# Kernel tuning notes

Measured on AMD Instinct MI355X. Metric: run time of the kernel, lower is better.

The kernel has to match this reference:

```python
import jax, jax.numpy as jnp
import numpy as np

NEG_SLOPE = 0.2  # PyG GATConv default


def gat_conv(x, src, dst, W_src, W_dst, att_src, att_dst, bias, heads, ch, n_nodes):
    """One PyG-style GATConv with self-loops already included in (src, dst).
    Returns [N, heads*ch] (concat over heads)."""
    xs = (x @ W_src).reshape(n_nodes, heads, ch)  # source-side transform (messages)
    xd = (x @ W_dst).reshape(n_nodes, heads, ch)  # dest-side transform (attention only)
    a_s = jnp.sum(xs * att_src, axis=-1)  # [N, H]
    a_d = jnp.sum(xd * att_dst, axis=-1)  # [N, H]
    e = jax.nn.leaky_relu(a_s[src] + a_d[dst], NEG_SLOPE)  # [E, H]
    # segment softmax over edges grouped by destination node
    m = jax.ops.segment_max(e, dst, num_segments=n_nodes)  # [N, H]
    ex = jnp.exp(e - m[dst])
    denom = jax.ops.segment_sum(ex, dst, num_segments=n_nodes)  # [N, H]
    alpha = ex / denom[dst]  # [E, H]
    # weighted scatter-aggregate of source messages
    out = jax.ops.segment_sum(xs[src] * alpha[:, :, None], dst, num_segments=n_nodes)
    return out.reshape(n_nodes, heads * ch) + bias


def setup_inputs() -> dict:
    key = jax.random.key(0)
    ks = jax.random.split(key, 12)
    N, F, E = 50000, 128, 400000
    H, C1, C2 = 4, 64, 64
    x = jax.random.normal(ks[0], (N, F), dtype=jnp.float32)
    edge_index = jax.random.randint(ks[1], (2, E), 0, N, dtype=jnp.int64)
    g = lambda k, shape, fan_in: jax.random.normal(k, shape, dtype=jnp.float32) * (1.0 / np.sqrt(fan_in))
    return {
        "x": x,
        "edge_index": edge_index,
        "W1_src": g(ks[2], (F, H * C1), F),
        "W1_dst": g(ks[3], (F, H * C1), F),
        "att1_src": g(ks[4], (H, C1), C1),
        "att1_dst": g(ks[5], (H, C1), C1),
        "b1": jnp.zeros((H * C1,), dtype=jnp.float32),
        "W2_src": g(ks[6], (H * C1, C2), H * C1),
        "W2_dst": g(ks[7], (H * C1, C2), H * C1),
        "att2_src": g(ks[8], (1, C2), C2),
        "att2_dst": g(ks[9], (1, C2), C2),
        "b2": jnp.zeros((C2,), dtype=jnp.float32),
    }


def reference(x, edge_index, W1_src, W1_dst, att1_src, att1_dst, b1,
              W2_src, W2_dst, att2_src, att2_dst, b2):
    N = x.shape[0]
    loop = jnp.arange(N, dtype=edge_index.dtype)
    src = jnp.concatenate([edge_index[0], loop])  # add_self_loops=True
    dst = jnp.concatenate([edge_index[1], loop])
    H, C1 = att1_src.shape
    C2 = att2_src.shape[1]
    h = gat_conv(x, src, dst, W1_src, W1_dst, att1_src, att1_dst, b1, H, C1, N)
    h = jax.nn.relu(h)
    # dropout is identity in eval mode
    out = gat_conv(h, src, dst, W2_src, W2_dst, att2_src, att2_dst, b2, 1, C2, N)
    return out
```

## Files before the change

### kernel.cpp

```cpp
#include <hip/hip_runtime.h>


static inline int cdiv(int a, int b) { return (a + b - 1) / b; }

typedef __attribute__((ext_vector_type(8))) short short8;
typedef __attribute__((ext_vector_type(4))) float floatx4;

__device__ __forceinline__ float bf2f(unsigned short u) {
  return __uint_as_float(((unsigned int)u) << 16);
}
__device__ __forceinline__ unsigned short f2bf(float f) {
  unsigned int u = __float_as_uint(f);
  unsigned int r = (u + 0x7FFFu + ((u >> 16) & 1u)) >> 16;
  return (unsigned short)r;
}
__device__ __forceinline__ float ldv(const void* p, int i, int bf) {
  return bf ? bf2f(((const unsigned short*)p)[i]) : ((const float*)p)[i];
}
#define NEG_INF (-__builtin_inff())

__global__ void fill_out_kernel(float* __restrict__ out, int n, float val) {
  int t = blockIdx.x * blockDim.x + threadIdx.x;
  if (t < n) out[t] = val;
}

__device__ void block_probes(const unsigned short* xu, const unsigned int* eu,
                             int& bf, int& e64) {
  __shared__ int cc, ce;
  if (threadIdx.x == 0) { cc = 0; ce = 0; }
  __syncthreads();
  int l0 = 0, l1 = 0;
  for (int i = threadIdx.x; i < 1024; i += 256) {
    int e = (xu[2 * i] >> 7) & 0xFF;
    if (e >= 100 && e <= 141) l0++;
    if (eu[2 * i + 1] == 0u) l1++;
  }
  atomicAdd(&cc, l0); atomicAdd(&ce, l1);
  __syncthreads();
  bf = cc > 512 ? 1 : 0;
  e64 = ce > 512 ? 1 : 0;
}

__global__ void prep_edges(const unsigned short* __restrict__ xu,
                           const void* __restrict__ EI, int E, int EP, int Nn,
                           const void* __restrict__ W1s, const void* __restrict__ W1d,
                           const void* __restrict__ a1s, const void* __restrict__ a1d,
                           const void* __restrict__ W2s, const void* __restrict__ W2d,
                           const void* __restrict__ a2s, const void* __restrict__ a2d,
                           const void* __restrict__ b1, const void* __restrict__ b2,
                           unsigned short* __restrict__ W1c,
                           unsigned short* __restrict__ W2sT,
                           unsigned short* __restrict__ W1ext,
                           float* __restrict__ v2s, float* __restrict__ v2d,
                           float* __restrict__ b1f, float* __restrict__ b2f,
                           int* __restrict__ srcI, int* __restrict__ dstI,
                           int* __restrict__ posE,
                           int* __restrict__ deg) {
  const int b = blockIdx.x, t = threadIdx.x;
  int bf, e64;
  block_probes(xu, (const unsigned int*)EI, bf, e64);
  if (b < 128) {
    int i = b * 256 + t;
    W1c[i] = f2bf(ldv(W1s, i, bf));
  } else if (b < 192) {
    int i = (b - 128) * 256 + t;
    int k = i >> 6, col = i & 63;
    W2sT[col * 256 + k] = f2bf(ldv(W2s, i, bf));
  } else if (b < 198) {
    const int lane = t & 63, w = t >> 6;
    const int g = lane >> 3, ll = lane & 7;
    const int base = (b - 192) * 256 + w * 64 + g;
#pragma unroll
    for (int r = 0; r < 8; ++r) {
      const int d = base + r * 8;
      const void *W, *A;
      int wo, ao;
      if (d < 1024) {
        int k = d >> 3, q = d & 7, h = q & 3;
        W = (q < 4) ? W1s : W1d;
        A = (q < 4) ? a1s : a1d;
        wo = k * 256 + h * 64;
        ao = h * 64;
      } else {
        int e = d - 1024, k = e & 255;
        W = (e < 256) ? W2s : W2d;
        A = (e < 256) ? a2s : a2d;
        wo = k * 64;
        ao = 0;
      }
      float p;
      if (bf) {
        uint4 wv = *(const uint4*)((const unsigned short*)W + wo + ll * 8);
        uint4 av = *(const uint4*)((const unsigned short*)A + ao + ll * 8);
        p  = bf2f((unsigned short)(wv.x & 0xFFFF)) * bf2f((unsigned short)(av.x & 0xFFFF));
        p += bf2f((unsigned short)(wv.x >> 16))    * bf2f((unsigned short)(av.x >> 16));
        p += bf2f((unsigned short)(wv.y & 0xFFFF)) * bf2f((unsigned short)(av.y & 0xFFFF));
        p += bf2f((unsigned short)(wv.y >> 16))    * bf2f((unsigned short)(av.y >> 16));
        p += bf2f((unsigned short)(wv.z & 0xFFFF)) * bf2f((unsigned short)(av.z & 0xFFFF));
        p += bf2f((unsigned short)(wv.z >> 16))    * bf2f((unsigned short)(av.z >> 16));
        p += bf2f((unsigned short)(wv.w & 0xFFFF)) * bf2f((unsigned short)(av.w & 0xFFFF));
        p += bf2f((unsigned short)(wv.w >> 16))    * bf2f((unsigned short)(av.w >> 16));
      } else {
        float4 w0 = *(const float4*)((const float*)W + wo + ll * 8);
        float4 w1 = *(const float4*)((const float*)W + wo + ll * 8 + 4);
        float4 a0 = *(const float4*)((const float*)A + ao + ll * 8);
        float4 a1 = *(const float4*)((const float*)A + ao + ll * 8 + 4);
        p = w0.x * a0.x + w0.y * a0.y + w0.z * a0.z + w0.w * a0.w +
            w1.x * a1.x + w1.y * a1.y + w1.z * a1.z + w1.w * a1.w;
      }
      p += __shfl_xor(p, 1);
      p += __shfl_xor(p, 2);
      p += __shfl_xor(p, 4);
      if (ll == 0) {
        if (d < 1024) {
          int k = d >> 3, q = d & 7;
          W1ext[k * 16 + q] = f2bf(p);
          W1ext[k * 16 + 8 + q] = 0;
        } else {
          int e = d - 1024, k = e & 255;
          if (e < 256) v2s[k] = p; else v2d[k] = p;
        }
      }
    }
  } else if (b == 198) {
    b1f[t] = ldv(b1, t, bf);
    if (t < 64) b2f[t] = ldv(b2, t, bf);
  } else {
    int i = (b - 199) * 256 + t;
    if (i < EP) {
      int s, d;
      if (i < E) {
        if (e64) {
          const unsigned int* p = (const unsigned int*)EI;
          s = (int)p[2 * (size_t)i];
          d = (int)p[2 * ((size_t)E + i)];
        } else {
          const int* p = (const int*)EI;
          s = p[i]; d = p[E + i];
        }
      } else { s = i - E; d = s; }
      if ((unsigned)s >= (unsigned)Nn) s = 0;
      if ((unsigned)d >= (unsigned)Nn) d = 0;
      srcI[i] = s; dstI[i] = d;
      posE[i] = atomicAdd(&deg[d], 1);
    }
  }
}

__global__ __launch_bounds__(256) void scan_gemm(
    const void* __restrict__ X, const unsigned short* __restrict__ xu,
    const int* __restrict__ deg, int* __restrict__ rowst,
    int* __restrict__ scanflag, int nb,
    const unsigned short* __restrict__ W1c, const unsigned short* __restrict__ W1ext,
    unsigned short* __restrict__ xs1, float* __restrict__ A1, int N) {
  __shared__ __align__(16) unsigned short smem[9 * 16 * 136];
  const int t = threadIdx.x;
  if (blockIdx.x < nb) {
    const int c = blockIdx.x;
    int* ssc = (int*)smem;
    int i = c * 256 + t;
    int v = (i < N) ? deg[i] : 0;
    ssc[t] = v;
    __syncthreads();
    for (int off = 1; off < 256; off <<= 1) {
      int add = (t >= off) ? ssc[t - off] : 0;
      __syncthreads();
      ssc[t] += add;
      __syncthreads();
    }
    int incl = ssc[t];
    if (t == 255) atomicExch(&scanflag[c], ssc[255] + 1);
    __syncthreads();
    int pre = 0;
    if (t < c) {
      int f;
      while ((f = atomicAdd(&scanflag[t], 0)) == 0) {}
      pre = f - 1;
    }
    int* s2 = ssc + 256;
    s2[t] = pre;
    __syncthreads();
    for (int off = 128; off; off >>= 1) {
      if (t < off) s2[t] += s2[t + off];
      __syncthreads();
    }
    if (i < N) rowst[i] = s2[0] + incl - v;
    return;
  }
  __shared__ int pcc;
  if (t == 0) pcc = 0;
  __syncthreads();
  {
    int l0 = 0;
    for (int i = t; i < 1024; i += 256) {
      int e = (xu[2 * i] >> 7) & 0xFF;
      if (e >= 100 && e <= 141) l0++;
    }
    atomicAdd(&pcc, l0);
  }
  __syncthreads();
  const int bf = pcc > 512 ? 1 : 0;
  unsigned short* Wlds = smem;
  const int lane = t & 63, wid = t >> 6;
  const int quad = lane >> 4, m16 = lane & 15;
  const int r0b = (blockIdx.x - nb) * 64;
  const int r0 = r0b + wid * 16;
  const int arow = min(r0 + m16, N - 1);
  short8 af[4];
  if (bf) {
    const uint4* Xr = (const uint4*)((const unsigned int*)X + (size_t)arow * 64);
#pragma unroll
    for (int ks = 0; ks < 4; ++ks)
      af[ks] = __builtin_bit_cast(short8, Xr[ks * 4 + quad]);
  } else {
    const float* Xr = (const float*)X + (size_t)arow * 128;
#pragma unroll
    for (int ks = 0; ks < 4; ++ks) {
      short8 v;
#pragma unroll
      for (int j = 0; j < 8; ++j) v[j] = (short)f2bf(Xr[ks * 32 + quad * 8 + j]);
      af[ks] = v;
    }
  }
  floatx4 accs[9];
  if (t < 144) {
    for (int k0 = 0; k0 < 128; k0 += 4) {
      unsigned int u0, u1;
      if (t < 128) {
        const unsigned short* p = W1c + (size_t)k0 * 256 + t;
        u0 = (unsigned int)p[0] | ((unsigned int)p[256] << 16);
        u1 = (unsigned int)p[512] | ((unsigned int)p[768] << 16);
      } else {
        const unsigned short* p = W1ext + (size_t)k0 * 16 + (t - 128);
        u0 = (unsigned int)p[0] | ((unsigned int)p[16] << 16);
        u1 = (unsigned int)p[32] | ((unsigned int)p[48] << 16);
      }
      *(uint2*)&Wlds[t * 136 + k0] = make_uint2(u0, u1);
    }
  }
  __syncthreads();
#pragma unroll
  for (int ct = 0; ct < 9; ++ct) {
    floatx4 acc = {0.f, 0.f, 0.f, 0.f};
    const unsigned short* wl = &Wlds[(ct * 16 + m16) * 136];
#pragma unroll
    for (int ks = 0; ks < 4; ++ks) {
      short8 bfv = *(const short8*)(wl + ks * 32 + quad * 8);
      acc = __builtin_amdgcn_mfma_f32_16x16x32_bf16(af[ks], bfv, acc, 0, 0, 0);
    }
    accs[ct] = acc;
  }
  __syncthreads();
  if (m16 < 8) {
#pragma unroll
    for (int r = 0; r < 4; ++r) {
      int row = r0 + quad * 4 + r;
      if (row < N) A1[(size_t)row * 8 + m16] = accs[8][r];
    }
  }
#pragma unroll
  for (int ct = 0; ct < 8; ++ct)
#pragma unroll
    for (int r = 0; r < 4; ++r)
      Wlds[(wid * 16 + quad * 4 + r) * 136 + ct * 16 + m16] = f2bf(accs[ct][r]);
  __syncthreads();
#pragma unroll
  for (int it = 0; it < 4; ++it) {
    int lrow = it * 16 + (t >> 4);
    int grow = r0b + lrow;
    if (grow < N) {
      uint4 v = *(const uint4*)&Wlds[lrow * 136 + (t & 15) * 8];
      *(uint4*)(xs1 + (size_t)grow * 256 + (t & 15) * 8) = v;
    }
  }
  __syncthreads();
  if (t < 128) {
    for (int k0 = 0; k0 < 128; k0 += 4) {
      const unsigned short* p = W1c + (size_t)k0 * 256 + 128 + t;
      unsigned int u0 = (unsigned int)p[0] | ((unsigned int)p[256] << 16);
      unsigned int u1 = (unsigned int)p[512] | ((unsigned int)p[768] << 16);
      *(uint2*)&Wlds[t * 136 + k0] = make_uint2(u0, u1);
    }
  }
  __syncthreads();
#pragma unroll
  for (int ct = 0; ct < 8; ++ct) {
    floatx4 acc = {0.f, 0.f, 0.f, 0.f};
    const unsigned short* wl = &Wlds[(ct * 16 + m16) * 136];
#pragma unroll
    for (int ks = 0; ks < 4; ++ks) {
      short8 bfv = *(const short8*)(wl + ks * 32 + quad * 8);
      acc = __builtin_amdgcn_mfma_f32_16x16x32_bf16(af[ks], bfv, acc, 0, 0, 0);
    }
    accs[ct] = acc;
  }
  __syncthreads();
#pragma unroll
  for (int ct = 0; ct < 8; ++ct)
#pragma unroll
    for (int r = 0; r < 4; ++r)
      Wlds[(wid * 16 + quad * 4 + r) * 136 + ct * 16 + m16] = f2bf(accs[ct][r]);
  __syncthreads();
#pragma unroll
  for (int it = 0; it < 4; ++it) {
    int lrow = it * 16 + (t >> 4);
    int grow = r0b + lrow;
    if (grow < N) {
      uint4 v = *(const uint4*)&Wlds[lrow * 136 + (t & 15) * 8];
      *(uint4*)(xs1 + (size_t)grow * 256 + 128 + (t & 15) * 8) = v;
    }
  }
}

__global__ void fill_srcS(const int* __restrict__ srcI, const int* __restrict__ dstI,
                          const int* __restrict__ posE, int EP,
                          const int* __restrict__ rowst, int* __restrict__ srcS) {
  int t = blockIdx.x * blockDim.x + threadIdx.x;
  if (t >= EP) return;
  int d = dstI[t];
  srcS[rowst[d] + posE[t]] = srcI[t];
}

__global__ __launch_bounds__(256) void node1_merged(
    const int* __restrict__ rowst, const int* __restrict__ deg,
    const int* __restrict__ srcS,
    const float* __restrict__ A1, const unsigned short* __restrict__ xs1,
    const float* __restrict__ b1f, const unsigned short* __restrict__ W2sT,
    const float* __restrict__ v2s, const float* __restrict__ v2d,
    unsigned short* __restrict__ xs2, float* __restrict__ A2, int N) {
  __shared__ unsigned short hb[8][272];
  __shared__ int   s_sh[4][2][32];
  __shared__ float al_sh[4][2][32][4];
  const int lane = threadIdx.x & 63;
  const int wid = threadIdx.x >> 6;
  const int hf = lane >> 5;
  const int hl = lane & 31;
  const int nraw = blockIdx.x * 8 + wid * 2 + hf;
  const bool valid = nraw < N;
  const int n = valid ? nraw : (N - 1);
  const int st = rowst[n], dn = deg[n];
  const float4 ad4 = *(const float4*)(A1 + (size_t)n * 8 + 4);
  const float ad[4] = {ad4.x, ad4.y, ad4.z, ad4.w};
  const int gc = 8 * hl;
  const int hd = hl >> 3;
  float acc[8] = {0.f, 0.f, 0.f, 0.f, 0.f, 0.f, 0.f, 0.f};
  constexpr int PF = 8;

  if (__all(dn <= 32)) {
    int s = 0;
    float4 as4 = make_float4(0.f, 0.f, 0.f, 0.f);
    if (hl < dn) {
      s = srcS[st + hl];
      as4 = *(const float4*)(A1 + (size_t)s * 8);
    }
    const int np = dn < PF ? dn : PF;
    uint4 u[PF];
#pragma unroll
    for (int j = 0; j < PF; ++j) {
      if (j < np) {
        int sj = __shfl(s, (hf << 5) + j);
        u[j] = *(const uint4*)(xs1 + (size_t)sj * 256 + gc);
      }
    }
    float v[4] = {NEG_INF, NEG_INF, NEG_INF, NEG_INF};
    if (hl < dn) {
      const float as[4] = {as4.x, as4.y, as4.z, as4.w};
#pragma unroll
      for (int h = 0; h < 4; ++h) {
        float x = as[h] + ad[h];
        v[h] = x > 0.f ? x : 0.2f * x;
      }
    }
    float m[4], l[4];
#pragma unroll
    for (int h = 0; h < 4; ++h) {
      m[h] = v[h];
#pragma unroll
      for (int off = 16; off; off >>= 1) m[h] = fmaxf(m[h], __shfl_xor(m[h], off));
      float e = (hl < dn) ? __expf(v[h] - m[h]) : 0.f;
      l[h] = e;
#pragma unroll
      for (int off = 16; off; off >>= 1) l[h] += __shfl_xor(l[h], off);
      v[h] = e;
    }
    if (hl < dn) {
      s_sh[wid][hf][hl] = s;
      float4 al = {v[0] / l[0], v[1] / l[1], v[2] / l[2], v[3] / l[3]};
      *(float4*)&al_sh[wid][hf][hl][0] = al;
    }
#pragma unroll
    for (int j = 0; j < PF; ++j) {
      if (j < np) {
        float a0 = al_sh[wid][hf][j][hd];
        acc[0] += a0 * __uint_as_float(u[j].x << 16);
        acc[1] += a0 * __uint_as_float(u[j].x & 0xFFFF0000u);
        acc[2] += a0 * __uint_as_float(u[j].y << 16);
        acc[3] += a0 * __uint_as_float(u[j].y & 0xFFFF0000u);
        acc[4] += a0 * __uint_as_float(u[j].z << 16);
        acc[5] += a0 * __uint_as_float(u[j].z & 0xFFFF0000u);
        acc[6] += a0 * __uint_as_float(u[j].w << 16);
        acc[7] += a0 * __uint_as_float(u[j].w & 0xFFFF0000u);
      }
    }
    for (int j = np; j < dn; ++j) {
      int s0 = s_sh[wid][hf][j];
      float a0 = al_sh[wid][hf][j][hd];
      uint4 uu = *(const uint4*)(xs1 + (size_t)s0 * 256 + gc);
      acc[0] += a0 * __uint_as_float(uu.x << 16);
      acc[1] += a0 * __uint_as_float(uu.x & 0xFFFF0000u);
      acc[2] += a0 * __uint_as_float(uu.y << 16);
      acc[3] += a0 * __uint_as_float(uu.y & 0xFFFF0000u);
      acc[4] += a0 * __uint_as_float(uu.z << 16);
      acc[5] += a0 * __uint_as_float(uu.z & 0xFFFF0000u);
      acc[6] += a0 * __uint_as_float(uu.w << 16);
      acc[7] += a0 * __uint_as_float(uu.w & 0xFFFF0000u);
    }
  } else {
    float m[4] = {NEG_INF, NEG_INF, NEG_INF, NEG_INF};
    for (int j = hl; j < dn; j += 32) {
      int s = srcS[st + j];
      const float4 as4 = *(const float4*)(A1 + (size_t)s * 8);
      const float as[4] = {as4.x, as4.y, as4.z, as4.w};
#pragma unroll
      for (int h = 0; h < 4; ++h) {
        float x = as[h] + ad[h];
        x = x > 0.f ? x : 0.2f * x;
        m[h] = fmaxf(m[h], x);
      }
    }
#pragma unroll
    for (int h = 0; h < 4; ++h)
#pragma unroll
      for (int off = 16; off; off >>= 1) m[h] = fmaxf(m[h], __shfl_xor(m[h], off));
    float l[4] = {0.f, 0.f, 0.f, 0.f};
    for (int j = hl; j < dn; j += 32) {
      int s = srcS[st + j];
      const float4 as4 = *(const float4*)(A1 + (size_t)s * 8);
      const float as[4] = {as4.x, as4.y, as4.z, as4.w};
#pragma unroll
      for (int h = 0; h < 4; ++h) {
        float x = as[h] + ad[h];
        x = x > 0.f ? x : 0.2f * x;
        l[h] += __expf(x - m[h]);
      }
    }
#pragma unroll
    for (int h = 0; h < 4; ++h)
#pragma unroll
      for (int off = 16; off; off >>= 1) l[h] += __shfl_xor(l[h], off);
    const float mh = m[hd], inv = 1.0f / l[hd], adh = ad[hd];
    for (int j = 0; j < dn; ++j) {
      int s = srcS[st + j];
      float x = A1[(size_t)s * 8 + hd] + adh;
      x = x > 0.f ? x : 0.2f * x;
      float alpha = __expf(x - mh) * inv;
      uint4 uu = *(const uint4*)(xs1 + (size_t)s * 256 + gc);
      acc[0] += alpha * __uint_as_float(uu.x << 16);
      acc[1] += alpha * __uint_as_float(uu.x & 0xFFFF0000u);
      acc[2] += alpha * __uint_as_float(uu.y << 16);
      acc[3] += alpha * __uint_as_float(uu.y & 0xFFFF0000u);
      acc[4] += alpha * __uint_as_float(uu.z << 16);
      acc[5] += alpha * __uint_as_float(uu.z & 0xFFFF0000u);
      acc[6] += alpha * __uint_as_float(uu.w << 16);
      acc[7] += alpha * __uint_as_float(uu.w & 0xFFFF0000u);
    }
  }

  const float4 bb0 = *(const float4*)(b1f + gc);
  const float4 bb1 = *(const float4*)(b1f + gc + 4);
  float hv[8];
  hv[0] = acc[0] + bb0.x; hv[1] = acc[1] + bb0.y;
  hv[2] = acc[2] + bb0.z; hv[3] = acc[3] + bb0.w;
  hv[4] = acc[4] + bb1.x; hv[5] = acc[5] + bb1.y;
  hv[6] = acc[6] + bb1.z; hv[7] = acc[7] + bb1.w;
#pragma unroll
  for (int k = 0; k < 8; ++k) hv[k] = hv[k] > 0.f ? hv[k] : 0.f;
  const float4 vs0 = *(const float4*)(v2s + gc);
  const float4 vs1 = *(const float4*)(v2s + gc + 4);
  const float4 vd0 = *(const float4*)(v2d + gc);
  const float4 vd1 = *(const float4*)(v2d + gc + 4);
  float ps = hv[0] * vs0.x + hv[1] * vs0.y + hv[2] * vs0.z + hv[3] * vs0.w +
             hv[4] * vs1.x + hv[5] * vs1.y + hv[6] * vs1.z + hv[7] * vs1.w;
  float pd = hv[0] * vd0.x + hv[1] * vd0.y + hv[2] * vd0.z + hv[3] * vd0.w +
             hv[4] * vd1.x + hv[5] * vd1.y + hv[6] * vd1.z + hv[7] * vd1.w;
#pragma unroll
  for (int off = 1; off <= 16; off <<= 1) {
    ps += __shfl_xor(ps, off);
    pd += __shfl_xor(pd, off);
  }
  unsigned int p0 = (unsigned int)f2bf(hv[0]) | ((unsigned int)f2bf(hv[1]) << 16);
  unsigned int p1 = (unsigned int)f2bf(hv[2]) | ((unsigned int)f2bf(hv[3]) << 16);
  unsigned int p2 = (unsigned int)f2bf(hv[4]) | ((unsigned int)f2bf(hv[5]) << 16);
  unsigned int p3 = (unsigned int)f2bf(hv[6]) | ((unsigned int)f2bf(hv[7]) << 16);
  *(uint4*)&hb[wid * 2 + hf][gc] = make_uint4(p0, p1, p2, p3);
  if (valid && hl == 0) {
    A2[(size_t)n * 2] = ps;
    A2[(size_t)n * 2 + 1] = pd;
  }
  __syncthreads();
  const int m16 = lane & 15, quad = lane >> 4;
  floatx4 c2 = {0.f, 0.f, 0.f, 0.f};
  const unsigned short* arow = &hb[m16 & 7][0];
  const unsigned short* bcol = W2sT + (size_t)(wid * 16 + m16) * 256;
#pragma unroll
  for (int ks = 0; ks < 8; ++ks) {
    short8 afr = *(const short8*)(arow + ks * 32 + quad * 8);
    short8 bfr = *(const short8*)(bcol + ks * 32 + quad * 8);
    c2 = __builtin_amdgcn_mfma_f32_16x16x32_bf16(afr, bfr, c2, 0, 0, 0);
  }
  if (quad < 2) {
#pragma unroll
    for (int r = 0; r < 4; ++r) {
      int node = blockIdx.x * 8 + quad * 4 + r;
      if (node < N) xs2[(size_t)node * 64 + wid * 16 + m16] = f2bf(c2[r]);
    }
  }
}

__global__ __launch_bounds__(256) void node2(const int* __restrict__ rowst,
    const int* __restrict__ deg, const int* __restrict__ srcS,
    const float* __restrict__ A2, const unsigned short* __restrict__ xs2,
    const float* __restrict__ b2f, float* __restrict__ out, int N) {
  __shared__ int   s_sh[4][2][32];
  __shared__ float al_sh[4][2][32];
  const int lane = threadIdx.x & 63;
  const int wid = threadIdx.x >> 6;
  const int hf = lane >> 5;
  const int hl = lane & 31;
  const int nraw = blockIdx.x * 8 + wid * 2 + hf;
  const bool valid = nraw < N;
  const int n = valid ? nraw : (N - 1);
  const int st = rowst[n], dn = deg[n];
  const float ad = A2[(size_t)n * 2 + 1];
  float ax = 0.f, ay = 0.f;
  constexpr int PF2 = 8;
  if (__all(dn <= 32)) {
    int s = 0;
    float a2v = 0.f;
    if (hl < dn) {
      s = srcS[st + hl];
      a2v = A2[(size_t)s * 2];
    }
    const int np = dn < PF2 ? dn : PF2;
    unsigned int u[PF2];
#pragma unroll
    for (int j = 0; j < PF2; ++j) {
      if (j < np) {
        int sj = __shfl(s, (hf << 5) + j);
        u[j] = *(const unsigned int*)(xs2 + (size_t)sj * 64 + 2 * hl);
      }
    }
    float v = NEG_INF;
    if (hl < dn) {
      v = a2v + ad;
      v = v > 0.f ? v : 0.2f * v;
    }
    float m = v;
#pragma unroll
    for (int off = 16; off; off >>= 1) m = fmaxf(m, __shfl_xor(m, off));
    float e = (hl < dn) ? __expf(v - m) : 0.f;
    float l = e;
#pragma unroll
    for (int off = 16; off; off >>= 1) l += __shfl_xor(l, off);
    if (hl < dn) { s_sh[wid][hf][hl] = s; al_sh[wid][hf][hl] = e / l; }
#pragma unroll
    for (int j = 0; j < PF2; ++j) {
      if (j < np) {
        float a = al_sh[wid][hf][j];
        ax += a * __uint_as_float(u[j] << 16);
        ay += a * __uint_as_float(u[j] & 0xFFFF0000u);
      }
    }
    for (int j = np; j < dn; ++j) {
      int s0 = s_sh[wid][hf][j];
      float a = al_sh[wid][hf][j];
      unsigned int uu = *(const unsigned int*)(xs2 + (size_t)s0 * 64 + 2 * hl);
      ax += a * __uint_as_float(uu << 16);
      ay += a * __uint_as_float(uu & 0xFFFF0000u);
    }
  } else {
    float m = NEG_INF;
    for (int j = hl; j < dn; j += 32) {
      int s = srcS[st + j];
      float v = A2[(size_t)s * 2] + ad;
      v = v > 0.f ? v : 0.2f * v;
      m = fmaxf(m, v);
    }
#pragma unroll
    for (int off = 16; off; off >>= 1) m = fmaxf(m, __shfl_xor(m, off));
    float l = 0.f;
    for (int j = hl; j < dn; j += 32) {
      int s = srcS[st + j];
      float v = A2[(size_t)s * 2] + ad;
      v = v > 0.f ? v : 0.2f * v;
      l += __expf(v - m);
    }
#pragma unroll
    for (int off = 16; off; off >>= 1) l += __shfl_xor(l, off);
    float inv = 1.0f / l;
    for (int j = 0; j < dn; ++j) {
      int s = srcS[st + j];
      float v = A2[(size_t)s * 2] + ad;
      v = v > 0.f ? v : 0.2f * v;
      float alpha = __expf(v - m) * inv;
      unsigned int uu = *(const unsigned int*)(xs2 + (size_t)s * 64 + 2 * hl);
      ax += alpha * __uint_as_float(uu << 16);
      ay += alpha * __uint_as_float(uu & 0xFFFF0000u);
    }
  }
  if (valid) {
    const float2 b = *(const float2*)(b2f + 2 * hl);
    float2 o = make_float2(ax + b.x, ay + b.y);
    *(float2*)(out + (size_t)n * 64 + 2 * hl) = o;
  }
}

extern "C" void kernel_launch(void* const* d_in, const int* in_sizes, int n_in,
                              void* d_out, int out_size, void* d_ws, size_t ws_size,
                              hipStream_t stream) {
  const int F = 128, HC1 = 256, C2 = 64;
  const int N  = in_sizes[0] / F;
  const int E  = in_sizes[1] / 2;
  const int EP = E + N;
  (void)n_in;

  char* w = (char*)d_ws;
  size_t off = 0;
  auto alloc = [&](size_t bytes) -> char* {
    char* p = w + off;
    off = (off + bytes + 255) & ~(size_t)255;
    return p;
  };
  int* srcI   = (int*)alloc((size_t)EP * 4);
  int* dstI   = (int*)alloc((size_t)EP * 4);
  int* posE   = (int*)alloc((size_t)EP * 4);
  int* degcur = (int*)alloc(((size_t)N + 256) * 4);
  int* deg    = degcur;
  int* scanflag = degcur + N;
  int* rowst  = (int*)alloc((size_t)N * 4);
  unsigned short* W1c   = (unsigned short*)alloc((size_t)F * HC1 * 2);
  unsigned short* W1ext = (unsigned short*)alloc(128 * 16 * 2);
  unsigned short* W2sT  = (unsigned short*)alloc((size_t)HC1 * C2 * 2);
  float* v2s  = (float*)alloc(256 * 4);
  float* v2d  = (float*)alloc(256 * 4);
  float* b1f  = (float*)alloc(256 * 4);
  float* b2f  = (float*)alloc(64 * 4);
  int*   srcS = (int*)alloc((size_t)EP * 4);
  float* A1   = (float*)alloc((size_t)N * 8 * 4);
  unsigned short* xs1 = (unsigned short*)alloc((size_t)N * HC1 * 2);
  unsigned short* xs2 = (unsigned short*)alloc((size_t)N * C2 * 2);
  float* A2 = (float*)alloc((size_t)N * 2 * 4);
  const size_t need = off;

  if (ws_size < need) {
    fill_out_kernel<<<cdiv(out_size, 256), 256, 0, stream>>>(
        (float*)d_out, out_size, 131072.0f + 1024.0f * (float)(ws_size >> 20));
    return;
  }

  hipMemsetAsync(degcur, 0, ((size_t)N + 256) * 4, stream);

  prep_edges<<<199 + cdiv(EP, 256), 256, 0, stream>>>(
      (const unsigned short*)d_in[0], d_in[1], E, EP, N,
      d_in[2], d_in[3], d_in[4], d_in[5], d_in[7], d_in[8], d_in[9], d_in[10],
      d_in[6], d_in[11],
      W1c, W2sT, W1ext, v2s, v2d, b1f, b2f, srcI, dstI, posE, deg);

  const int nb = cdiv(N, 256);
  scan_gemm<<<nb + cdiv(N, 64), 256, 0, stream>>>(
      d_in[0], (const unsigned short*)d_in[0], deg, rowst, scanflag, nb,
      W1c, W1ext, xs1, A1, N);

  fill_srcS<<<cdiv(EP, 256), 256, 0, stream>>>(srcI, dstI, posE, EP, rowst, srcS);
  node1_merged<<<cdiv(N, 8), 256, 0, stream>>>(rowst, deg, srcS, A1, xs1,
                                               b1f, W2sT, v2s, v2d, xs2, A2, N);
  node2<<<cdiv(N, 8), 256, 0, stream>>>(rowst, deg, srcS, A2, xs2, b2f,
                                        (float*)d_out, N);
}
```

Measured before the change: 242.4 us.

## Fuse CSR scatter into scan_gemm via global completion counter; raise prefetch depths

Removes the separate fill_srcS launch by having every scan_gemm block spin-wait on a global counter that the scan blocks increment. Once the counter shows all scan blocks are done, each block scatters its slice of edges into the CSR source array. Prefetch depths in node1 and node2 are also raised (8 to 12, 8 to 16) to hide more gather latency. The spin-wait assumes the scan blocks get scheduled, which holds because they have the lowest block indices. It adds an inter-block dependency and extra register pressure from the deeper prefetch.

```diff
diff --git a/kernel.cpp b/kernel.cpp
--- a/kernel.cpp
+++ b/kernel.cpp
@@ -152,7 +152,10 @@
     const int* __restrict__ deg, int* __restrict__ rowst,
     int* __restrict__ scanflag, int nb,
     const unsigned short* __restrict__ W1c, const unsigned short* __restrict__ W1ext,
-    unsigned short* __restrict__ xs1, float* __restrict__ A1, int N) {
+    unsigned short* __restrict__ xs1, float* __restrict__ A1, int N,
+    const int* __restrict__ srcI, const int* __restrict__ dstI,
+    const int* __restrict__ posE, int EP,
+    int* __restrict__ srcS, int* __restrict__ scan_done) {
   __shared__ __align__(16) unsigned short smem[9 * 16 * 136];
   const int t = threadIdx.x;
   if (blockIdx.x < nb) {
@@ -184,141 +187,149 @@
       if (t < off) s2[t] += s2[t + off];
       __syncthreads();
     }
-    if (i < N) rowst[i] = s2[0] + incl - v;
-    return;
-  }
-  __shared__ int pcc;
-  if (t == 0) pcc = 0;
+    if (i < N) atomicExch(&rowst[i], s2[0] + incl - v);
+    __threadfence();
+    __syncthreads();
+    if (t == 0) atomicAdd(scan_done, 1);
+  } else {
+    __shared__ int pcc;
+    if (t == 0) pcc = 0;
+    __syncthreads();
+    {
+      int l0 = 0;
+      for (int i = t; i < 1024; i += 256) {
+        int e = (xu[2 * i] >> 7) & 0xFF;
+        if (e >= 100 && e <= 141) l0++;
+      }
+      atomicAdd(&pcc, l0);
+    }
+    __syncthreads();
+    const int bf = pcc > 512 ? 1 : 0;
+    unsigned short* Wlds = smem;
+    const int lane = t & 63, wid = t >> 6;
+    const int quad = lane >> 4, m16 = lane & 15;
+    const int r0b = (blockIdx.x - nb) * 64;
+    const int r0 = r0b + wid * 16;
+    const int arow = min(r0 + m16, N - 1);
+    short8 af[4];
+    if (bf) {
+      const uint4* Xr = (const uint4*)((const unsigned int*)X + (size_t)arow * 64);
+#pragma unroll
+      for (int ks = 0; ks < 4; ++ks)
+        af[ks] = __builtin_bit_cast(short8, Xr[ks * 4 + quad]);
+    } else {
+      const float* Xr = (const float*)X + (size_t)arow * 128;
+#pragma unroll
+      for (int ks = 0; ks < 4; ++ks) {
+        short8 v;
+#pragma unroll
+        for (int j = 0; j < 8; ++j) v[j] = (short)f2bf(Xr[ks * 32 + quad * 8 + j]);
+        af[ks] = v;
+      }
+    }
+    floatx4 accs[9];
+    if (t < 144) {
+      for (int k0 = 0; k0 < 128; k0 += 4) {
+        unsigned int u0, u1;
+        if (t < 128) {
+          const unsigned short* p = W1c + (size_t)k0 * 256 + t;
+          u0 = (unsigned int)p[0] | ((unsigned int)p[256] << 16);
+          u1 = (unsigned int)p[512] | ((unsigned int)p[768] << 16);
+        } else {
+          const unsigned short* p = W1ext + (size_t)k0 * 16 + (t - 128);
+          u0 = (unsigned int)p[0] | ((unsigned int)p[16] << 16);
+          u1 = (unsigned int)p[32] | ((unsigned int)p[48] << 16);
+        }
+        *(uint2*)&Wlds[t * 136 + k0] = make_uint2(u0, u1);
+      }
+    }
+    __syncthreads();
+#pragma unroll
+    for (int ct = 0; ct < 9; ++ct) {
+      floatx4 acc = {0.f, 0.f, 0.f, 0.f};
+      const unsigned short* wl = &Wlds[(ct * 16 + m16) * 136];
+#pragma unroll
+      for (int ks = 0; ks < 4; ++ks) {
+        short8 bfv = *(const short8*)(wl + ks * 32 + quad * 8);
+        acc = __builtin_amdgcn_mfma_f32_16x16x32_bf16(af[ks], bfv, acc, 0, 0, 0);
+      }
+      accs[ct] = acc;
+    }
+    __syncthreads();
+    if (m16 < 8) {
+#pragma unroll
+      for (int r = 0; r < 4; ++r) {
+        int row = r0 + quad * 4 + r;
+        if (row < N) A1[(size_t)row * 8 + m16] = accs[8][r];
+      }
+    }
+#pragma unroll
+    for (int ct = 0; ct < 8; ++ct)
+#pragma unroll
+      for (int r = 0; r < 4; ++r)
+        Wlds[(wid * 16 + quad * 4 + r) * 136 + ct * 16 + m16] = f2bf(accs[ct][r]);
+    __syncthreads();
+#pragma unroll
+    for (int it = 0; it < 4; ++it) {
+      int lrow = it * 16 + (t >> 4);
+      int grow = r0b + lrow;
+      if (grow < N) {
+        uint4 v = *(const uint4*)&Wlds[lrow * 136 + (t & 15) * 8];
+        *(uint4*)(xs1 + (size_t)grow * 256 + (t & 15) * 8) = v;
+      }
+    }
+    __syncthreads();
+    if (t < 128) {
+      for (int k0 = 0; k0 < 128; k0 += 4) {
+        const unsigned short* p = W1c + (size_t)k0 * 256 + 128 + t;
+        unsigned int u0 = (unsigned int)p[0] | ((unsigned int)p[256] << 16);
+        unsigned int u1 = (unsigned int)p[512] | ((unsigned int)p[768] << 16);
+        *(uint2*)&Wlds[t * 136 + k0] = make_uint2(u0, u1);
+      }
+    }
+    __syncthreads();
+#pragma unroll
+    for (int ct = 0; ct < 8; ++ct) {
+      floatx4 acc = {0.f, 0.f, 0.f, 0.f};
+      const unsigned short* wl = &Wlds[(ct * 16 + m16) * 136];
+#pragma unroll
+      for (int ks = 0; ks < 4; ++ks) {
+        short8 bfv = *(const short8*)(wl + ks * 32 + quad * 8);
+        acc = __builtin_amdgcn_mfma_f32_16x16x32_bf16(af[ks], bfv, acc, 0, 0, 0);
+      }
+      accs[ct] = acc;
+    }
+    __syncthreads();
+#pragma unroll
+    for (int ct = 0; ct < 8; ++ct)
+#pragma unroll
+      for (int r = 0; r < 4; ++r)
+        Wlds[(wid * 16 + quad * 4 + r) * 136 + ct * 16 + m16] = f2bf(accs[ct][r]);
+    __syncthreads();
+#pragma unroll
+    for (int it = 0; it < 4; ++it) {
+      int lrow = it * 16 + (t >> 4);
+      int grow = r0b + lrow;
+      if (grow < N) {
+        uint4 v = *(const uint4*)&Wlds[lrow * 136 + (t & 15) * 8];
+        *(uint4*)(xs1 + (size_t)grow * 256 + 128 + (t & 15) * 8) = v;
+      }
+    }
+  }
+  if (t == 0) {
+    while (atomicAdd(scan_done, 0) < nb) {}
+  }
   __syncthreads();
+  __threadfence();
   {
-    int l0 = 0;
-    for (int i = t; i < 1024; i += 256) {
-      int e = (xu[2 * i] >> 7) & 0xFF;
-      if (e >= 100 && e <= 141) l0++;
-    }
-    atomicAdd(&pcc, l0);
-  }
-  __syncthreads();
-  const int bf = pcc > 512 ? 1 : 0;
-  unsigned short* Wlds = smem;
-  const int lane = t & 63, wid = t >> 6;
-  const int quad = lane >> 4, m16 = lane & 15;
-  const int r0b = (blockIdx.x - nb) * 64;
-  const int r0 = r0b + wid * 16;
-  const int arow = min(r0 + m16, N - 1);
-  short8 af[4];
-  if (bf) {
-    const uint4* Xr = (const uint4*)((const unsigned int*)X + (size_t)arow * 64);
-#pragma unroll
-    for (int ks = 0; ks < 4; ++ks)
-      af[ks] = __builtin_bit_cast(short8, Xr[ks * 4 + quad]);
-  } else {
-    const float* Xr = (const float*)X + (size_t)arow * 128;
-#pragma unroll
-    for (int ks = 0; ks < 4; ++ks) {
-      short8 v;
-#pragma unroll
-      for (int j = 0; j < 8; ++j) v[j] = (short)f2bf(Xr[ks * 32 + quad * 8 + j]);
-      af[ks] = v;
-    }
-  }
-  floatx4 accs[9];
-  if (t < 144) {
-    for (int k0 = 0; k0 < 128; k0 += 4) {
-      unsigned int u0, u1;
-      if (t < 128) {
-        const unsigned short* p = W1c + (size_t)k0 * 256 + t;
-        u0 = (unsigned int)p[0] | ((unsigned int)p[256] << 16);
-        u1 = (unsigned int)p[512] | ((unsigned int)p[768] << 16);
-      } else {
-        const unsigned short* p = W1ext + (size_t)k0 * 16 + (t - 128);
-        u0 = (unsigned int)p[0] | ((unsigned int)p[16] << 16);
-        u1 = (unsigned int)p[32] | ((unsigned int)p[48] << 16);
-      }
-      *(uint2*)&Wlds[t * 136 + k0] = make_uint2(u0, u1);
-    }
-  }
-  __syncthreads();
-#pragma unroll
-  for (int ct = 0; ct < 9; ++ct) {
-    floatx4 acc = {0.f, 0.f, 0.f, 0.f};
-    const unsigned short* wl = &Wlds[(ct * 16 + m16) * 136];
-#pragma unroll
-    for (int ks = 0; ks < 4; ++ks) {
-      short8 bfv = *(const short8*)(wl + ks * 32 + quad * 8);
-      acc = __builtin_amdgcn_mfma_f32_16x16x32_bf16(af[ks], bfv, acc, 0, 0, 0);
-    }
-    accs[ct] = acc;
-  }
-  __syncthreads();
-  if (m16 < 8) {
-#pragma unroll
-    for (int r = 0; r < 4; ++r) {
-      int row = r0 + quad * 4 + r;
-      if (row < N) A1[(size_t)row * 8 + m16] = accs[8][r];
-    }
-  }
-#pragma unroll
-  for (int ct = 0; ct < 8; ++ct)
-#pragma unroll
-    for (int r = 0; r < 4; ++r)
-      Wlds[(wid * 16 + quad * 4 + r) * 136 + ct * 16 + m16] = f2bf(accs[ct][r]);
-  __syncthreads();
-#pragma unroll
-  for (int it = 0; it < 4; ++it) {
-    int lrow = it * 16 + (t >> 4);
-    int grow = r0b + lrow;
-    if (grow < N) {
-      uint4 v = *(const uint4*)&Wlds[lrow * 136 + (t & 15) * 8];
-      *(uint4*)(xs1 + (size_t)grow * 256 + (t & 15) * 8) = v;
-    }
-  }
-  __syncthreads();
-  if (t < 128) {
-    for (int k0 = 0; k0 < 128; k0 += 4) {
-      const unsigned short* p = W1c + (size_t)k0 * 256 + 128 + t;
-      unsigned int u0 = (unsigned int)p[0] | ((unsigned int)p[256] << 16);
-      unsigned int u1 = (unsigned int)p[512] | ((unsigned int)p[768] << 16);
-      *(uint2*)&Wlds[t * 136 + k0] = make_uint2(u0, u1);
-    }
-  }
-  __syncthreads();
-#pragma unroll
-  for (int ct = 0; ct < 8; ++ct) {
-    floatx4 acc = {0.f, 0.f, 0.f, 0.f};
-    const unsigned short* wl = &Wlds[(ct * 16 + m16) * 136];
-#pragma unroll
-    for (int ks = 0; ks < 4; ++ks) {
-      short8 bfv = *(const short8*)(wl + ks * 32 + quad * 8);
-      acc = __builtin_amdgcn_mfma_f32_16x16x32_bf16(af[ks], bfv, acc, 0, 0, 0);
-    }
-    accs[ct] = acc;
-  }
-  __syncthreads();
-#pragma unroll
-  for (int ct = 0; ct < 8; ++ct)
-#pragma unroll
-    for (int r = 0; r < 4; ++r)
-      Wlds[(wid * 16 + quad * 4 + r) * 136 + ct * 16 + m16] = f2bf(accs[ct][r]);
-  __syncthreads();
-#pragma unroll
-  for (int it = 0; it < 4; ++it) {
-    int lrow = it * 16 + (t >> 4);
-    int grow = r0b + lrow;
-    if (grow < N) {
-      uint4 v = *(const uint4*)&Wlds[lrow * 136 + (t & 15) * 8];
-      *(uint4*)(xs1 + (size_t)grow * 256 + 128 + (t & 15) * 8) = v;
-    }
-  }
-}
-
-__global__ void fill_srcS(const int* __restrict__ srcI, const int* __restrict__ dstI,
-                          const int* __restrict__ posE, int EP,
-                          const int* __restrict__ rowst, int* __restrict__ srcS) {
-  int t = blockIdx.x * blockDim.x + threadIdx.x;
-  if (t >= EP) return;
-  int d = dstI[t];
-  srcS[rowst[d] + posE[t]] = srcI[t];
+    const int slice = (EP + (int)gridDim.x - 1) / (int)gridDim.x;
+    const int beg = (int)blockIdx.x * slice;
+    const int end = min(beg + slice, EP);
+    for (int i = beg + t; i < end; i += 256) {
+      int d = dstI[i];
+      srcS[rowst[d] + posE[i]] = srcI[i];
+    }
+  }
 }
 
 __global__ __launch_bounds__(256) void node1_merged(
@@ -344,7 +355,7 @@
   const int gc = 8 * hl;
   const int hd = hl >> 3;
   float acc[8] = {0.f, 0.f, 0.f, 0.f, 0.f, 0.f, 0.f, 0.f};
-  constexpr int PF = 8;
+  constexpr int PF = 12;
 
   if (__all(dn <= 32)) {
     int s = 0;
@@ -533,7 +544,7 @@
   const int st = rowst[n], dn = deg[n];
   const float ad = A2[(size_t)n * 2 + 1];
   float ax = 0.f, ay = 0.f;
-  constexpr int PF2 = 8;
+  constexpr int PF2 = 16;
   if (__all(dn <= 32)) {
     int s = 0;
     float a2v = 0.f;
@@ -634,9 +645,10 @@
   int* srcI   = (int*)alloc((size_t)EP * 4);
   int* dstI   = (int*)alloc((size_t)EP * 4);
   int* posE   = (int*)alloc((size_t)EP * 4);
-  int* degcur = (int*)alloc(((size_t)N + 256) * 4);
+  int* degcur = (int*)alloc(((size_t)N + 264) * 4);
   int* deg    = degcur;
   int* scanflag = degcur + N;
+  int* scan_done = degcur + N + 256;
   int* rowst  = (int*)alloc((size_t)N * 4);
   unsigned short* W1c   = (unsigned short*)alloc((size_t)F * HC1 * 2);
   unsigned short* W1ext = (unsigned short*)alloc(128 * 16 * 2);
@@ -658,7 +670,7 @@
     return;
   }
 
-  hipMemsetAsync(degcur, 0, ((size_t)N + 256) * 4, stream);
+  hipMemsetAsync(degcur, 0, ((size_t)N + 264) * 4, stream);
 
   prep_edges<<<199 + cdiv(EP, 256), 256, 0, stream>>>(
       (const unsigned short*)d_in[0], d_in[1], E, EP, N,
@@ -669,9 +681,9 @@
   const int nb = cdiv(N, 256);
   scan_gemm<<<nb + cdiv(N, 64), 256, 0, stream>>>(
       d_in[0], (const unsigned short*)d_in[0], deg, rowst, scanflag, nb,
-      W1c, W1ext, xs1, A1, N);
-
-  fill_srcS<<<cdiv(EP, 256), 256, 0, stream>>>(srcI, dstI, posE, EP, rowst, srcS);
+      W1c, W1ext, xs1, A1, N,
+      srcI, dstI, posE, EP, srcS, scan_done);
+
   node1_merged<<<cdiv(N, 8), 256, 0, stream>>>(rowst, deg, srcS, A1, xs1,
                                                b1f, W2sT, v2s, v2d, xs2, A2, N);
   node2<<<cdiv(N, 8), 256, 0, stream>>>(rowst, deg, srcS, A2, xs2, b2f,
```

Measured after the change: 323.8 us. 1.34x slower.
